# Kernel tuning notes

Measured on AMD Instinct MI355X. Metric: run time of the kernel, lower is better.

## Reference

```python
import jax, jax.numpy as jnp
import numpy as np

B, T, D = 2, 4096, 512
H = 8
HD = D // H


def setup_inputs() -> dict:
    key = jax.random.key(0)
    ks = jax.random.split(key, 6)
    s = 0.02
    return {
        "token_embed": jax.random.normal(ks[0], (B, T, D), jnp.float32),
        "Wq": jax.random.normal(ks[1], (D, D), jnp.float32) * s,
        "Wk": jax.random.normal(ks[2], (D, D), jnp.float32) * s,
        "Wv": jax.random.normal(ks[3], (D, D), jnp.float32) * s,
        "Wo": jax.random.normal(ks[4], (D, D), jnp.float32) * s,
        "bo": jnp.zeros((D,), jnp.float32),
    }


def reference(token_embed, Wq, Wk, Wv, Wo, bo):
    b, t, d_in = token_embed.shape
    # QKV projections (Linear without bias): x @ W^T with W stored [d_out, d_in]
    q = jnp.einsum("btd,ed->bte", token_embed, Wq).reshape(b, t, H, HD).transpose(0, 2, 1, 3)
    k = jnp.einsum("btd,ed->bte", token_embed, Wk).reshape(b, t, H, HD).transpose(0, 2, 1, 3)
    v = jnp.einsum("btd,ed->bte", token_embed, Wv).reshape(b, t, H, HD).transpose(0, 2, 1, 3)
    # Scores [b, h, t, t] with causal mask applied before scaling (as in source)
    scores = jnp.einsum("bhqd,bhkd->bhqk", q, k)
    causal = jnp.tril(jnp.ones((t, t), bool))  # True = keep
    scores = jnp.where(causal, scores, -jnp.inf)
    attn = jax.nn.softmax(scores / jnp.sqrt(jnp.float32(HD)), axis=-1)
    # dropout p=0.0 -> identity
    ctx = jnp.einsum("bhqk,bhkd->bhqd", attn, v)
    ctx = ctx.transpose(0, 2, 1, 3).reshape(b, t, H * HD)
    return jnp.einsum("btd,ed->bte", ctx, Wo) + bo
```

## Files before the change

### kernel.cpp

```cpp
#include <hip/hip_runtime.h>

#define B_  2
#define T_  4096
#define D_  512
#define H_  8
#define HD_ 64
#define M_  (B_*T_)

typedef _Float16 h16;
typedef _Float16 v8h __attribute__((ext_vector_type(8)));
typedef _Float16 h2  __attribute__((ext_vector_type(2)));
typedef float v4f __attribute__((ext_vector_type(4)));
typedef unsigned short us;
typedef unsigned short us8 __attribute__((ext_vector_type(8)));

union PaU { v8h v; h2 p[4]; };

#define AS1 __attribute__((address_space(1)))
#define AS3 __attribute__((address_space(3)))

__device__ __forceinline__ float bf2f(us u){
  union { unsigned int i; float f; } v; v.i = ((unsigned int)u) << 16; return v.f;
}
__device__ __forceinline__ us f2bf(float f){
  union { float f; unsigned int u; } v; v.f = f;
  unsigned int r = v.u + 0x7FFFu + ((v.u >> 16) & 1u);
  return (us)(r >> 16);
}
__device__ __forceinline__ v4f zero4(){ v4f z; z[0]=0.f; z[1]=0.f; z[2]=0.f; z[3]=0.f; return z; }

__device__ __forceinline__ void glds16(const h16* g, h16* l){
  __builtin_amdgcn_global_load_lds((const AS1 int*)(const void*)g,
                                   (AS3 int*)(void*)l, 16, 0, 0);
}

__device__ __forceinline__ h2 pkrtz(float a, float b){
  auto t = __builtin_amdgcn_cvt_pkrtz(a, b);
  h2 r; __builtin_memcpy(&r, &t, sizeof(r)); return r;
}

#define MFMA32 __builtin_amdgcn_mfma_f32_16x16x32_f16

__global__ __launch_bounds__(256) void conv_all(
    const void* __restrict__ x, const void* __restrict__ w0, const void* __restrict__ w1,
    const void* __restrict__ w2, const void* __restrict__ w3, const void* __restrict__ bo,
    h16* __restrict__ xb, h16* __restrict__ d0, h16* __restrict__ d1,
    h16* __restrict__ d2, h16* __restrict__ d3, float* __restrict__ bof)
{
  const int bid = blockIdx.x, tid = threadIdx.x;
  const void* src; int e0; int seg;
  h16* dst = nullptr;
  if (bid < 2048)      { src = x; e0 = bid * 2048; dst = xb; seg = 0; }
  else if (bid < 2560) {
    const int wsel = (bid - 2048) >> 7;
    src = (wsel == 0) ? w0 : (wsel == 1) ? w1 : (wsel == 2) ? w2 : w3;
    dst = (wsel == 0) ? d0 : (wsel == 1) ? d1 : (wsel == 2) ? d2 : d3;
    e0 = ((bid - 2048) & 127) * 2048; seg = 0;
  } else                { src = bo; e0 = 0; seg = 1; }

  __shared__ int sflag;
  if (tid == 0) sflag = 0;
  __syncthreads();
  const float probe = bf2f(((const us*)src)[e0 + tid]);
  if (!(fabsf(probe) < 1e4f)) atomicAdd(&sflag, 1);
  __syncthreads();
  const int isf32 = (sflag != 0);

  if (seg) {
    if (tid < 64) {
      const int i = tid * 8;
#pragma unroll
      for (int e = 0; e < 8; e++)
        bof[i + e] = isf32 ? ((const float*)src)[i + e] : bf2f(((const us*)src)[i + e]);
    }
    return;
  }
  const int i = e0 + tid * 8;
  float v[8];
  if (isf32) {
    const float* pf = (const float*)src + i;
    const float4 a = *(const float4*)pf;
    const float4 c = *(const float4*)(pf + 4);
    v[0]=a.x; v[1]=a.y; v[2]=a.z; v[3]=a.w; v[4]=c.x; v[5]=c.y; v[6]=c.z; v[7]=c.w;
  } else {
    const us8 u = *(const us8*)((const us*)src + i);
#pragma unroll
    for (int e = 0; e < 8; e++) v[e] = bf2f(u[e]);
  }
  v8h o;
#pragma unroll
  for (int e = 0; e < 8; e++) o[e] = (h16)v[e];
  *(v8h*)(dst + i) = o;
}

__device__ __forceinline__ void stage4(const h16* __restrict__ A, const h16* __restrict__ W,
                                       int m0, int n0, int kk, h16* sA, h16* sB, int tid){
  const int colA = (tid & 3) << 3;
  const int rowT = tid >> 2;
#pragma unroll
  for (int rd = 0; rd < 2; rd++) {
    const int row = rd * 64 + rowT;
    const int f = rd * 2048 + tid * 8;
    glds16(A + (size_t)(m0 + row) * D_ + kk + colA, sA + f);
    glds16(W + (size_t)(n0 + row) * D_ + kk + colA, sB + f);
  }
}

__device__ __forceinline__ void gemm_core(const h16* __restrict__ A,
                                          const h16* __restrict__ W,
                                          int m0, int n0, h16* sA, h16* sB,
                                          v4f acc[4][4]) {
  const int tid = threadIdx.x;
  const int lane = tid & 63, wid = tid >> 6;
  const int r = lane & 15, q = lane >> 4;
#pragma unroll
  for (int i = 0; i < 4; i++)
#pragma unroll
    for (int j = 0; j < 4; j++) acc[i][j] = zero4();

  stage4(A, W, m0, n0, 0, sA, sB, tid);
#pragma unroll 1
  for (int kt = 0; kt < 16; kt++) {
    if (kt < 15) {
      const int nb = (kt + 1) & 1;
      stage4(A, W, m0, n0, (kt + 1) * 32, sA + nb * 4096, sB + nb * 4096, tid);
      asm volatile("s_waitcnt vmcnt(4)" ::: "memory");
    } else {
      asm volatile("s_waitcnt vmcnt(0)" ::: "memory");
    }
    asm volatile("s_barrier" ::: "memory");
    const h16* pA = sA + (kt & 1) * 4096 + ((wid & 1) * 64 + r) * 32 + q * 8;
    const h16* pB = sB + (kt & 1) * 4096 + ((wid >> 1) * 64 + r) * 32 + q * 8;
    v8h a[4], b[4];
#pragma unroll
    for (int i = 0; i < 4; i++) a[i] = *(const v8h*)(pA + i * 512);
#pragma unroll
    for (int j = 0; j < 4; j++) b[j] = *(const v8h*)(pB + j * 512);
#pragma unroll
    for (int i = 0; i < 4; i++)
#pragma unroll
      for (int j = 0; j < 4; j++)
        acc[i][j] = MFMA32(a[i], b[j], acc[i][j], 0, 0, 0);
    asm volatile("s_barrier" ::: "memory");
  }
}

__global__ __launch_bounds__(256, 3) void gemm_qkv(
    const h16* __restrict__ X,
    const h16* __restrict__ Wq, const h16* __restrict__ Wk, const h16* __restrict__ Wv,
    h16* __restrict__ Qo, h16* __restrict__ Ko, h16* __restrict__ VTo)
{
  __shared__ h16 sA[2 * 4096], sB[2 * 4096];
  const h16* W = (blockIdx.z == 0) ? Wq : (blockIdx.z == 1 ? Wk : Wv);
  const int m0 = blockIdx.x * 128, n0 = blockIdx.y * 128;
  v4f acc[4][4];
  gemm_core(X, W, m0, n0, sA, sB, acc);
  const int lane = threadIdx.x & 63, wid = threadIdx.x >> 6;
  const int r = lane & 15, q = lane >> 4;
  const int wm = m0 + (wid & 1) * 64, wn = n0 + (wid >> 1) * 64;
  if (blockIdx.z == 2) {
#pragma unroll
    for (int i = 0; i < 4; i++)
#pragma unroll
      for (int j = 0; j < 4; j++)
#pragma unroll
        for (int rr = 0; rr < 4; rr++) {
          const int row = wm + i*16 + q*4 + rr;
          const int col = wn + j*16 + r;
          const int bb = row >> 12, tt = row & (T_ - 1);
          const int hh = col >> 6,  hd = col & 63;
          const int t6 = tt & 63;
          const int tperm = (tt & ~63) | (t6 & 3) | (((t6 >> 2) & 3) << 3)
                          | (((t6 >> 4) & 1) << 2) | (t6 & 32);
          VTo[((size_t)(((bb << 3) + hh) << 6) + hd) * T_ + tperm] = (h16)acc[i][j][rr];
        }
  } else {
    h16* Y = (blockIdx.z == 0) ? Qo : Ko;
    const float sc = (blockIdx.z == 0) ? 0.1803368801f : 1.0f;
#pragma unroll
    for (int i = 0; i < 4; i++)
#pragma unroll
      for (int j = 0; j < 4; j++)
#pragma unroll
        for (int rr = 0; rr < 4; rr++)
          Y[(size_t)(wm + i*16 + q*4 + rr) * D_ + wn + j*16 + r] = (h16)(acc[i][j][rr] * sc);
  }
}

__global__ __launch_bounds__(256, 3) void gemm_out(
    const h16* __restrict__ A, const h16* __restrict__ W,
    const float* __restrict__ bias, void* __restrict__ out, const void* __restrict__ xprobe)
{
  __shared__ h16 sA[2 * 4096], sB[2 * 4096];
  __shared__ int sflag;
  if (threadIdx.x == 0) sflag = 0;
  __syncthreads();
  const float probe = bf2f(((const us*)xprobe)[threadIdx.x]);
  if (!(fabsf(probe) < 1e4f)) atomicAdd(&sflag, 1);
  __syncthreads();
  const int flag = (sflag != 0);

  const int m0 = blockIdx.x * 128, n0 = blockIdx.y * 128;
  v4f acc[4][4];
  gemm_core(A, W, m0, n0, sA, sB, acc);
  const int lane = threadIdx.x & 63, wid = threadIdx.x >> 6;
  const int r = lane & 15, q = lane >> 4;
  const int wm = m0 + (wid & 1) * 64, wn = n0 + (wid >> 1) * 64;
#pragma unroll
  for (int i = 0; i < 4; i++)
#pragma unroll
    for (int j = 0; j < 4; j++)
#pragma unroll
      for (int rr = 0; rr < 4; rr++) {
        const int row = wm + i*16 + q*4 + rr;
        const int col = wn + j*16 + r;
        const float v = acc[i][j][rr] + bias[col];
        if (flag) ((float*)out)[(size_t)row * D_ + col] = v;
        else ((us*)out)[(size_t)row * D_ + col] = f2bf(v);
      }
}

__global__ __launch_bounds__(256, 4) void attn_kernel(
    const h16* __restrict__ Q, const h16* __restrict__ K,
    const h16* __restrict__ VT, h16* __restrict__ Ctx)
{
  const int h = blockIdx.x;
  const int pos = blockIdx.y + (blockIdx.z << 6);
  const int qc = 63 - (pos >> 1);
  const int b  = pos & 1;
  const int tid = threadIdx.x;
  const int wid = tid >> 6, lane = tid & 63;
  const int r = lane & 15, quad = lane >> 4;
  const int kw = wid & 1, qw = wid >> 1;

  const size_t headoff = (size_t)b * T_ * D_ + (size_t)h * HD_;
  const h16* Qh  = Q + headoff;
  const h16* Kh  = K + headoff;
  const h16* VTh = VT + (size_t)(b * H_ + h) * HD_ * T_;
  h16* Ch = Ctx + headoff;

  __shared__ h16 smem[4][4096];

  const int q0 = qc * 64 + qw * 32;
  const int ntiles = qc + 1;

  const v8h aq00 = *(const v8h*)(Qh + (size_t)(q0 + r) * D_ + quad * 8);
  const v8h aq01 = *(const v8h*)(Qh + (size_t)(q0 + r) * D_ + 32 + quad * 8);
  const v8h aq10 = *(const v8h*)(Qh + (size_t)(q0 + 16 + r) * D_ + quad * 8);
  const v8h aq11 = *(const v8h*)(Qh + (size_t)(q0 + 16 + r) * D_ + 32 + quad * 8);

  v8h vone;
#pragma unroll
  for (int e = 0; e < 8; e++) vone[e] = (h16)1;

  v4f o0[4], o1[4];
#pragma unroll
  for (int j = 0; j < 4; j++) { o0[j] = zero4(); o1[j] = zero4(); }
  v4f ld0 = zero4(), ld1 = zero4();

  const int srow = tid >> 3;
  const int sj = (tid & 7) ^ (srow & 7);
  const h16* kcur = Kh + (size_t)srow * D_ + sj * 8;
  const h16* vcur = VTh + (size_t)srow * T_ + sj * 8;

  glds16(kcur, &smem[0][tid * 8]); glds16(kcur + 32 * D_, &smem[0][2048 + tid * 8]);
  glds16(vcur, &smem[2][tid * 8]); glds16(vcur + 32 * T_, &smem[2][2048 + tid * 8]);
  kcur += 64 * D_; vcur += 64;

  const int xo0 = (quad ^ (r & 7)) * 8;
  const int xo1 = ((quad + 4) ^ (r & 7)) * 8;
  const int xov = ((quad + kw * 4) ^ (r & 7)) * 8;
  const int krow = kw * 32 + r;
  const int kloc = kw * 32 + quad * 4;
  const int qlim0 = qw * 32 + r, qlim1 = qw * 32 + 16 + r;

#define ATT_TILE(CB, MASKED) do {                                              \
    const h16* sKc = smem[(CB)];                                               \
    const h16* sVc = smem[2 + (CB)];                                           \
    const h16* bK = sKc + krow * 64;                                           \
    const v8h ka0 = *(const v8h*)(bK + xo0);                                   \
    const v8h ka1 = *(const v8h*)(bK + xo1);                                   \
    const v8h ka2 = *(const v8h*)(bK + 16 * 64 + xo0);                         \
    const v8h ka3 = *(const v8h*)(bK + 16 * 64 + xo1);                         \
    v8h va[4];                                                                 \
    _Pragma("unroll")                                                          \
    for (int j = 0; j < 4; j++)                                                \
      va[j] = *(const v8h*)(sVc + (j * 16 + r) * 64 + xov);                    \
    v4f s00 = zero4(), s10 = zero4(), s01 = zero4(), s11 = zero4();            \
    __builtin_amdgcn_s_setprio(1);                                             \
    s00 = MFMA32(ka0, aq00, s00, 0,0,0); s00 = MFMA32(ka1, aq01, s00, 0,0,0);  \
    s10 = MFMA32(ka2, aq00, s10, 0,0,0); s10 = MFMA32(ka3, aq01, s10, 0,0,0);  \
    s01 = MFMA32(ka0, aq10, s01, 0,0,0); s01 = MFMA32(ka1, aq11, s01, 0,0,0);  \
    s11 = MFMA32(ka2, aq10, s11, 0,0,0); s11 = MFMA32(ka3, aq11, s11, 0,0,0);  \
    __builtin_amdgcn_s_setprio(0);                                             \
    PaU pa0, pa1;                                                              \
    _Pragma("unroll")                                                          \
    for (int qb = 0; qb < 2; qb++) {                                           \
      const v4f& sa = qb ? s01 : s00;                                          \
      const v4f& sb = qb ? s11 : s10;                                          \
      const int qlim = qb ? qlim1 : qlim0;                                     \
      float e0[4], e1[4];                                                      \
      _Pragma("unroll")                                                        \
      for (int rr = 0; rr < 4; rr++) {                                         \
        float v0 = sa[rr], v1 = sb[rr];                                        \
        if (MASKED) {                                                          \
          if (kloc + rr > qlim)      v0 = -1e30f;                              \
          if (kloc + 16 + rr > qlim) v1 = -1e30f;                              \
        }                                                                      \
        e0[rr] = exp2f(v0); e1[rr] = exp2f(v1);                                \
      }                                                                        \
      PaU* pa = qb ? &pa1 : &pa0;                                              \
      pa->p[0] = pkrtz(e0[0], e0[1]); pa->p[1] = pkrtz(e0[2], e0[3]);          \
      pa->p[2] = pkrtz(e1[0], e1[1]); pa->p[3] = pkrtz(e1[2], e1[3]);          \
    }                                                                          \
    __builtin_amdgcn_s_setprio(1);                                             \
    ld0 = MFMA32(pa0.v, vone, ld0, 0,0,0);                                     \
    ld1 = MFMA32(pa1.v, vone, ld1, 0,0,0);                                     \
    _Pragma("unroll")                                                          \
    for (int j = 0; j < 4; j++) {                                              \
      o0[j] = MFMA32(pa0.v, va[j], o0[j], 0,0,0);                              \
      o1[j] = MFMA32(pa1.v, va[j], o1[j], 0,0,0);                              \
    }                                                                          \
    __builtin_amdgcn_s_setprio(0);                                             \
  } while(0)

#pragma unroll 1
  for (int kt = 0; kt < ntiles - 1; kt++) {
    asm volatile("s_waitcnt vmcnt(0)" ::: "memory");
    asm volatile("s_barrier" ::: "memory");
    const int nb = (kt + 1) & 1;
    glds16(kcur, &smem[nb][tid * 8]);
    glds16(kcur + 32 * D_, &smem[nb][2048 + tid * 8]);
    glds16(vcur, &smem[2 + nb][tid * 8]);
    glds16(vcur + 32 * T_, &smem[2 + nb][2048 + tid * 8]);
    kcur += 64 * D_; vcur += 64;
    ATT_TILE(kt & 1, false);
  }
  asm volatile("s_waitcnt vmcnt(0)" ::: "memory");
  asm volatile("s_barrier" ::: "memory");
  ATT_TILE((ntiles - 1) & 1, true);
#undef ATT_TILE

  __syncthreads();
  float* const red = (float*)&smem[0][0];
  float* const seg = red + qw * 2112;
  float* const lred = red + 4224;
  if (kw) {
#pragma unroll
    for (int hdb = 0; hdb < 4; hdb++)
#pragma unroll
      for (int j = 0; j < 4; j++) {
        seg[(quad * 4 + j) * 66 + hdb * 16 + r] = o0[hdb][j];
        seg[(16 + quad * 4 + j) * 66 + hdb * 16 + r] = o1[hdb][j];
      }
    if (r == 0) {
#pragma unroll
      for (int j = 0; j < 4; j++) {
        lred[qw * 32 + quad * 4 + j] = ld0[j];
        lred[qw * 32 + 16 + quad * 4 + j] = ld1[j];
      }
    }
  }
  __syncthreads();
  if (!kw) {
    float inv0[4], inv1[4];
#pragma unroll
    for (int j = 0; j < 4; j++) {
      inv0[j] = 1.0f / (ld0[j] + lred[qw * 32 + quad * 4 + j]);
      inv1[j] = 1.0f / (ld1[j] + lred[qw * 32 + 16 + quad * 4 + j]);
    }
#pragma unroll
    for (int hdb = 0; hdb < 4; hdb++)
#pragma unroll
      for (int j = 0; j < 4; j++) {
        const float a0 = o0[hdb][j] + seg[(quad * 4 + j) * 66 + hdb * 16 + r];
        const float a1 = o1[hdb][j] + seg[(16 + quad * 4 + j) * 66 + hdb * 16 + r];
        Ch[(size_t)(q0 + quad * 4 + j) * D_ + hdb * 16 + r] = (h16)(a0 * inv0[j]);
        Ch[(size_t)(q0 + 16 + quad * 4 + j) * D_ + hdb * 16 + r] = (h16)(a1 * inv1[j]);
      }
  }
}

extern "C" void kernel_launch(void* const* d_in, const int* in_sizes, int n_in,
                              void* d_out, int out_size, void* d_ws, size_t ws_size,
                              hipStream_t stream) {
  char* ws = (char*)d_ws;
  h16* xb  = (h16*)(ws + 0);
  h16* qb  = (h16*)(ws + 8388608);
  h16* kb  = (h16*)(ws + 16777216);
  h16* vt  = (h16*)(ws + 25165824);
  h16* ctx = (h16*)(ws + 33554432);
  h16* wqb = (h16*)(ws + 41943040);
  h16* wkb = (h16*)(ws + 41943040 + 524288);
  h16* wvb = (h16*)(ws + 41943040 + 2 * 524288);
  h16* wob = (h16*)(ws + 41943040 + 3 * 524288);
  float* bof = (float*)(ws + 41943040 + 4 * 524288);

  conv_all<<<2561, 256, 0, stream>>>(d_in[0], d_in[1], d_in[2], d_in[3], d_in[4],
                                     d_in[5], xb, wqb, wkb, wvb, wob, bof);
  gemm_qkv<<<dim3(M_ / 128, D_ / 128, 3), 256, 0, stream>>>(xb, wqb, wkb, wvb, qb, kb, vt);
  attn_kernel<<<dim3(H_, 64, B_), 256, 0, stream>>>(qb, kb, vt, ctx);
  gemm_out<<<dim3(M_ / 128, D_ / 128, 1), 256, 0, stream>>>(ctx, wob, bof, d_out, d_in[0]);
}
```

Before: 170.1 us.

## Triple-buffer K/V tiles in attention kernel with two-deep prefetch

```diff
diff --git a/kernel.cpp b/kernel.cpp
--- a/kernel.cpp
+++ b/kernel.cpp
@@ -220,7 +220,7 @@
       }
 }
 
-__global__ __launch_bounds__(256, 4) void attn_kernel(
+__global__ __launch_bounds__(256, 3) void attn_kernel(
     const h16* __restrict__ Q, const h16* __restrict__ K,
     const h16* __restrict__ VT, h16* __restrict__ Ctx)
 {
@@ -239,7 +239,7 @@
   const h16* VTh = VT + (size_t)(b * H_ + h) * HD_ * T_;
   h16* Ch = Ctx + headoff;
 
-  __shared__ h16 smem[4][4096];
+  __shared__ h16 smem[6][4096];
 
   const int q0 = qc * 64 + qw * 32;
   const int ntiles = qc + 1;
@@ -263,9 +263,16 @@
   const h16* kcur = Kh + (size_t)srow * D_ + sj * 8;
   const h16* vcur = VTh + (size_t)srow * T_ + sj * 8;
 
-  glds16(kcur, &smem[0][tid * 8]); glds16(kcur + 32 * D_, &smem[0][2048 + tid * 8]);
-  glds16(vcur, &smem[2][tid * 8]); glds16(vcur + 32 * T_, &smem[2][2048 + tid * 8]);
-  kcur += 64 * D_; vcur += 64;
+#define STAGE(BUF) do {                                                        \
+    glds16(kcur, &smem[(BUF)][tid * 8]);                                       \
+    glds16(kcur + 32 * D_, &smem[(BUF)][2048 + tid * 8]);                      \
+    glds16(vcur, &smem[3 + (BUF)][tid * 8]);                                   \
+    glds16(vcur + 32 * T_, &smem[3 + (BUF)][2048 + tid * 8]);                  \
+    kcur += 64 * D_; vcur += 64;                                               \
+  } while(0)
+
+  STAGE(0);
+  if (ntiles > 1) STAGE(1);
 
   const int xo0 = (quad ^ (r & 7)) * 8;
   const int xo1 = ((quad + 4) ^ (r & 7)) * 8;
@@ -276,7 +283,7 @@
 
 #define ATT_TILE(CB, MASKED) do {                                              \
     const h16* sKc = smem[(CB)];                                               \
-    const h16* sVc = smem[2 + (CB)];                                           \
+    const h16* sVc = smem[3 + (CB)];                                           \
     const h16* bK = sKc + krow * 64;                                           \
     const v8h ka0 = *(const v8h*)(bK + xo0);                                   \
     const v8h ka1 = *(const v8h*)(bK + xo1);                                   \
@@ -324,22 +331,24 @@
     __builtin_amdgcn_s_setprio(0);                                             \
   } while(0)
 
+  int cb = 0;
 #pragma unroll 1
-  for (int kt = 0; kt < ntiles - 1; kt++) {
-    asm volatile("s_waitcnt vmcnt(0)" ::: "memory");
+  for (int kt = 0; kt < ntiles; kt++) {
+    if (kt + 1 < ntiles) {
+      asm volatile("s_waitcnt vmcnt(4)" ::: "memory");
+    } else {
+      asm volatile("s_waitcnt vmcnt(0)" ::: "memory");
+    }
     asm volatile("s_barrier" ::: "memory");
-    const int nb = (kt + 1) & 1;
-    glds16(kcur, &smem[nb][tid * 8]);
-    glds16(kcur + 32 * D_, &smem[nb][2048 + tid * 8]);
-    glds16(vcur, &smem[2 + nb][tid * 8]);
-    glds16(vcur + 32 * T_, &smem[2 + nb][2048 + tid * 8]);
-    kcur += 64 * D_; vcur += 64;
-    ATT_TILE(kt & 1, false);
-  }
-  asm volatile("s_waitcnt vmcnt(0)" ::: "memory");
-  asm volatile("s_barrier" ::: "memory");
-  ATT_TILE((ntiles - 1) & 1, true);
+    if (kt + 2 < ntiles) {
+      const int nb = (cb + 2 >= 3) ? (cb - 1) : (cb + 2);
+      STAGE(nb);
+    }
+    ATT_TILE(cb, kt == ntiles - 1);
+    cb = (cb == 2) ? 0 : cb + 1;
+  }
 #undef ATT_TILE
+#undef STAGE
 
   __syncthreads();
   float* const red = (float*)&smem[0][0];
```

New measurement: 179.1 us. +5.3%, slower.
